# Kernel tuning notes

Hardware: AMD Instinct MI355X
Metric: run time of the kernel (lower is better)

Reference implementation:

```python
import jax, jax.numpy as jnp
import numpy as np

H = 1024
V = 50257
S = 4096
L = 2


def gru_cell(x, h, Wih, Whh, bih, bhh):
    # x: (1, in), h: (1, H); PyTorch GRUCell math
    gi = x @ Wih.T + bih  # (1, 3H)
    gh = h @ Whh.T + bhh  # (1, 3H)
    i_r, i_z, i_n = jnp.split(gi, 3, axis=1)
    h_r, h_z, h_n = jnp.split(gh, 3, axis=1)
    r = jax.nn.sigmoid(i_r + h_r)
    z = jax.nn.sigmoid(i_z + h_z)
    n = jnp.tanh(i_n + r * h_n)
    return (1.0 - z) * n + z * h


def setup_inputs() -> dict:
    key = jax.random.key(0)
    ks = jax.random.split(key, 16)
    s = 0.02
    inp = {
        "input": jax.random.randint(ks[0], (1,), 0, V),
        "last_context": jax.random.normal(ks[1], (1, H), jnp.float32),
        "hidden": jax.random.normal(ks[2], (L, 1, H), jnp.float32),
        "encoder_outputs": jax.random.normal(ks[3], (S, 1, H), jnp.float32),
        "emb": jax.random.normal(ks[4], (V, H), jnp.float32) * s,
        "attn_W": jax.random.normal(ks[5], (H, H), jnp.float32) * s,
        "attn_b": jnp.zeros((H,), jnp.float32),
        "Wih0": jax.random.normal(ks[6], (3 * H, 2 * H), jnp.float32) * s,
        "Whh0": jax.random.normal(ks[7], (3 * H, H), jnp.float32) * s,
        "bih0": jnp.zeros((3 * H,), jnp.float32),
        "bhh0": jnp.zeros((3 * H,), jnp.float32),
        "Wih1": jax.random.normal(ks[8], (3 * H, H), jnp.float32) * s,
        "Whh1": jax.random.normal(ks[9], (3 * H, H), jnp.float32) * s,
        "bih1": jnp.zeros((3 * H,), jnp.float32),
        "bhh1": jnp.zeros((3 * H,), jnp.float32),
        "out_W": jax.random.normal(ks[10], (V, 2 * H), jnp.float32) * s,
        "out_b": jnp.zeros((V,), jnp.float32),
    }
    return inp


def reference(input, last_context, hidden, encoder_outputs, emb, attn_W, attn_b,
              Wih0, Whh0, bih0, bhh0, Wih1, Whh1, bih1, bhh1, out_W, out_b):
    # Embedding lookup for the single decoded token -> (1, H)
    x = emb[input].reshape(1, H)
    rnn_in = jnp.concatenate([x, last_context], axis=1)  # (1, 2H)
    # Stacked 2-layer GRU, single timestep
    h0 = gru_cell(rnn_in, hidden[0], Wih0, Whh0, bih0, bhh0)  # (1, H)
    h1 = gru_cell(h0, hidden[1], Wih1, Whh1, bih1, bhh1)      # (1, H)
    new_hidden = jnp.stack([h0, h1], axis=0)                  # (L, 1, H)
    rnn_output = h1                                           # (1, H)
    # Additive-score attention, vectorized over all S encoder timesteps
    enc = encoder_outputs[:, 0, :]                            # (S, H)
    energies = (enc @ attn_W.T + attn_b) @ rnn_output[0]      # (S,)
    attn_w = jax.nn.softmax(energies)                         # (S,)
    context = (attn_w @ enc).reshape(1, H)                    # (1, H)
    logits = jnp.concatenate([rnn_output, context], axis=1) @ out_W.T + out_b
    output = jax.nn.log_softmax(logits, axis=-1)              # (1, V)
    return output, context, new_hidden, attn_w.reshape(1, 1, S)
```

## Files before the change

kernel.cpp:

```cpp
#include <hip/hip_runtime.h>
#include <math.h>

static constexpr int kH = 1024;
static constexpr int kV = 50257;
static constexpr int kS = 4096;
static constexpr int kLogitsBlocks = (kV + 3) / 4;

__device__ __forceinline__ float wred_sum(float v) {
#pragma unroll
  for (int o = 32; o > 0; o >>= 1) v += __shfl_down(v, o, 64);
  return v;
}
__device__ __forceinline__ float wred_max(float v) {
#pragma unroll
  for (int o = 32; o > 0; o >>= 1) v = fmaxf(v, __shfl_down(v, o, 64));
  return v;
}

__global__ __launch_bounds__(256) void gru_kernel(
    const int* __restrict__ tok, const float* __restrict__ emb,
    const float* __restrict__ xa, const float* __restrict__ xb,
    const float* __restrict__ hprev,
    const float* __restrict__ Wih, const float* __restrict__ Whh,
    const float* __restrict__ bih, const float* __restrict__ bhh,
    float* __restrict__ hout, float* __restrict__ hout2,
    float* __restrict__ zu, float* __restrict__ zc) {
  const int i = blockIdx.x;
  const int t = threadIdx.x;
  const int lane = t & 63, wid = t >> 6;

  if (zu) {
    if (i < 4) zu[i * 256 + t] = 0.f;
    else if (i < 8) zc[(i - 4) * 256 + t] = 0.f;
  }

  const float* xrow = tok ? (emb + (size_t)tok[0] * kH) : xa;
  const int nk4 = tok ? 512 : 256;
  const size_t xw = tok ? (size_t)(2 * kH) : (size_t)kH;

  const float4* X0 = (const float4*)xrow;
  const float4* X1 = (const float4*)xb;
  const float4* Wr = (const float4*)(Wih + (size_t)i * xw);
  const float4* Wz = (const float4*)(Wih + (size_t)(kH + i) * xw);
  const float4* Wn = (const float4*)(Wih + (size_t)(2 * kH + i) * xw);
  const float4* Ur = (const float4*)(Whh + (size_t)i * kH);
  const float4* Uz = (const float4*)(Whh + (size_t)(kH + i) * kH);
  const float4* Un = (const float4*)(Whh + (size_t)(2 * kH + i) * kH);
  const float4* Hp = (const float4*)hprev;

  float ar = 0.f, az = 0.f, an = 0.f, br = 0.f, bz = 0.f, bn = 0.f;
  for (int k = t; k < nk4; k += 256) {
    const float4 x = (k < 256) ? X0[k] : X1[k - 256];
    float4 w;
    w = Wr[k]; ar += w.x * x.x + w.y * x.y + w.z * x.z + w.w * x.w;
    w = Wz[k]; az += w.x * x.x + w.y * x.y + w.z * x.z + w.w * x.w;
    w = Wn[k]; an += w.x * x.x + w.y * x.y + w.z * x.z + w.w * x.w;
  }
  {
    const float4 h = Hp[t];
    float4 w;
    w = Ur[t]; br += w.x * h.x + w.y * h.y + w.z * h.z + w.w * h.w;
    w = Uz[t]; bz += w.x * h.x + w.y * h.y + w.z * h.z + w.w * h.w;
    w = Un[t]; bn += w.x * h.x + w.y * h.y + w.z * h.z + w.w * h.w;
  }
  ar = wred_sum(ar); az = wred_sum(az); an = wred_sum(an);
  br = wred_sum(br); bz = wred_sum(bz); bn = wred_sum(bn);
  __shared__ float red[6][4];
  if (lane == 0) {
    red[0][wid] = ar; red[1][wid] = az; red[2][wid] = an;
    red[3][wid] = br; red[4][wid] = bz; red[5][wid] = bn;
  }
  __syncthreads();
  if (t == 0) {
    const float s0 = red[0][0] + red[0][1] + red[0][2] + red[0][3];
    const float s1 = red[1][0] + red[1][1] + red[1][2] + red[1][3];
    const float s2 = red[2][0] + red[2][1] + red[2][2] + red[2][3];
    const float s3 = red[3][0] + red[3][1] + red[3][2] + red[3][3];
    const float s4 = red[4][0] + red[4][1] + red[4][2] + red[4][3];
    const float s5 = red[5][0] + red[5][1] + red[5][2] + red[5][3];
    const float r = 1.f / (1.f + expf(-((s0 + bih[i]) + (s3 + bhh[i]))));
    const float z = 1.f / (1.f + expf(-((s1 + bih[kH + i]) + (s4 + bhh[kH + i]))));
    const float n = tanhf((s2 + bih[2 * kH + i]) + r * (s5 + bhh[2 * kH + i]));
    const float h = (1.f - z) * n + z * hprev[i];
    hout[i] = h;
    hout2[i] = h;
  }
}

__global__ __launch_bounds__(256) void attn_u_kernel(
    const float* __restrict__ attn_W, const float* __restrict__ h1,
    float* __restrict__ u) {
  const int t = threadIdx.x;
  const int j0 = blockIdx.x * 8;
  const float4* W4 = (const float4*)attn_W;
  float4 acc = make_float4(0.f, 0.f, 0.f, 0.f);
#pragma unroll
  for (int j = j0; j < j0 + 8; ++j) {
    const float hj = h1[j];
    const float4 w = W4[(size_t)j * 256 + t];
    acc.x += hj * w.x; acc.y += hj * w.y; acc.z += hj * w.z; acc.w += hj * w.w;
  }
  atomicAdd(&u[4 * t + 0], acc.x);
  atomicAdd(&u[4 * t + 1], acc.y);
  atomicAdd(&u[4 * t + 2], acc.z);
  atomicAdd(&u[4 * t + 3], acc.w);
}

__global__ __launch_bounds__(256) void energies_kernel(
    const float* __restrict__ enc, const float* __restrict__ u,
    float* __restrict__ e) {
  const int lane = threadIdx.x & 63;
  const int s = blockIdx.x * 4 + (threadIdx.x >> 6);
  const float4* E = (const float4*)(enc + (size_t)s * kH);
  const float4* U = (const float4*)u;
  float acc = 0.f;
#pragma unroll
  for (int k = lane; k < 256; k += 64) {
    const float4 a = E[k], b = U[k];
    acc += a.x * b.x + a.y * b.y + a.z * b.z + a.w * b.w;
  }
  acc = wred_sum(acc);
  if (lane == 0) e[s] = acc;
}

__global__ __launch_bounds__(1024) void softmax4096_kernel(
    float* __restrict__ e, float* __restrict__ o_attn) {
  const int t = threadIdx.x;
  const int lane = t & 63, wid = t >> 6;
  __shared__ float red[16];
  __shared__ float bc;
  const float4 v = ((const float4*)e)[t];
  float m = fmaxf(fmaxf(v.x, v.y), fmaxf(v.z, v.w));
  m = wred_max(m);
  if (lane == 0) red[wid] = m;
  __syncthreads();
  if (t == 0) {
    float mm = red[0];
    for (int w = 1; w < 16; ++w) mm = fmaxf(mm, red[w]);
    bc = mm;
  }
  __syncthreads();
  const float M = bc;
  const float e0 = expf(v.x - M), e1 = expf(v.y - M);
  const float e2 = expf(v.z - M), e3 = expf(v.w - M);
  float ssum = e0 + e1 + e2 + e3;
  ssum = wred_sum(ssum);
  if (lane == 0) red[wid] = ssum;
  __syncthreads();
  if (t == 0) {
    float tt = 0.f;
    for (int w = 0; w < 16; ++w) tt += red[w];
    bc = 1.f / tt;
  }
  __syncthreads();
  const float inv = bc;
  const float4 r4 = make_float4(e0 * inv, e1 * inv, e2 * inv, e3 * inv);
  ((float4*)e)[t] = r4;
  o_attn[4 * t + 0] = r4.x;
  o_attn[4 * t + 1] = r4.y;
  o_attn[4 * t + 2] = r4.z;
  o_attn[4 * t + 3] = r4.w;
}

__global__ __launch_bounds__(256) void context_kernel(
    const float* __restrict__ enc, const float* __restrict__ w,
    float* __restrict__ ctx) {
  const int t = threadIdx.x;
  const int s0 = blockIdx.x * 32;
  const float4* E = (const float4*)enc;
  float4 acc = make_float4(0.f, 0.f, 0.f, 0.f);
#pragma unroll 4
  for (int s = s0; s < s0 + 32; ++s) {
    const float ws = w[s];
    const float4 e = E[(size_t)s * 256 + t];
    acc.x += ws * e.x; acc.y += ws * e.y; acc.z += ws * e.z; acc.w += ws * e.w;
  }
  atomicAdd(&ctx[4 * t + 0], acc.x);
  atomicAdd(&ctx[4 * t + 1], acc.y);
  atomicAdd(&ctx[4 * t + 2], acc.z);
  atomicAdd(&ctx[4 * t + 3], acc.w);
}

__global__ __launch_bounds__(256) void logits_kernel(
    const float* __restrict__ out_W, const float* __restrict__ out_b,
    const float* __restrict__ h1, const float* __restrict__ ctx,
    float* __restrict__ logits, float* __restrict__ part) {
  const int lane = threadIdx.x & 63;
  const int wid = threadIdx.x >> 6;
  const int v = blockIdx.x * 4 + wid;
  __shared__ float lvals[4];

  float val = -INFINITY;
  if (v < kV) {
    const float4* W = (const float4*)(out_W + (size_t)v * (2 * kH));
    const float4* X0 = (const float4*)h1;
    const float4* X1 = (const float4*)ctx;
    float acc = 0.f;
#pragma unroll
    for (int k = lane; k < 512; k += 64) {
      const float4 w = W[k];
      const float4 x = (k < 256) ? X0[k] : X1[k - 256];
      acc += w.x * x.x + w.y * x.y + w.z * x.z + w.w * x.w;
    }
    acc = wred_sum(acc);
    val = acc + out_b[v];
    if (lane == 0) logits[v] = val;
  }
  if (lane == 0) lvals[wid] = val;
  __syncthreads();
  if (threadIdx.x == 0) {
    const float m = fmaxf(fmaxf(lvals[0], lvals[1]), fmaxf(lvals[2], lvals[3]));
    float s = 0.f;
#pragma unroll
    for (int w = 0; w < 4; ++w)
      if (lvals[w] != -INFINITY) s += expf(lvals[w] - m);
    part[2 * blockIdx.x] = m;
    part[2 * blockIdx.x + 1] = s;
  }
}

__global__ __launch_bounds__(1024) void lse_combine_kernel(
    const float* __restrict__ part, float* __restrict__ stats) {
  const int t = threadIdx.x;
  const int lane = t & 63, wid = t >> 6;
  __shared__ float red[16];
  __shared__ float bc;
  float m = -INFINITY;
  for (int b = t; b < kLogitsBlocks; b += 1024) m = fmaxf(m, part[2 * b]);
  m = wred_max(m);
  if (lane == 0) red[wid] = m;
  __syncthreads();
  if (t == 0) {
    float mm = red[0];
    for (int w = 1; w < 16; ++w) mm = fmaxf(mm, red[w]);
    bc = mm;
  }
  __syncthreads();
  const float M = bc;
  float s = 0.f;
  for (int b = t; b < kLogitsBlocks; b += 1024)
    s += part[2 * b + 1] * expf(part[2 * b] - M);
  s = wred_sum(s);
  if (lane == 0) red[wid] = s;
  __syncthreads();
  if (t == 0) {
    float tt = 0.f;
    for (int w = 0; w < 16; ++w) tt += red[w];
    stats[0] = M;
    stats[1] = logf(tt);
  }
}

__global__ __launch_bounds__(256) void finalize_kernel(
    float* __restrict__ logits, const float* __restrict__ stats,
    const float* __restrict__ ctx_ws, float* __restrict__ o_ctx) {
  const int v = blockIdx.x * 256 + threadIdx.x;
  if (v < kV) logits[v] -= (stats[0] + stats[1]);
  if (v < kH) o_ctx[v] = ctx_ws[v];
}

extern "C" void kernel_launch(void* const* d_in, const int* in_sizes, int n_in,
                              void* d_out, int out_size, void* d_ws,
                              size_t ws_size, hipStream_t stream) {
  const int* tok = (const int*)d_in[0];
  const float* last_ctx = (const float*)d_in[1];
  const float* hidden = (const float*)d_in[2];
  const float* enc = (const float*)d_in[3];
  const float* emb = (const float*)d_in[4];
  const float* attn_W = (const float*)d_in[5];
  const float* Wih0 = (const float*)d_in[7];
  const float* Whh0 = (const float*)d_in[8];
  const float* bih0 = (const float*)d_in[9];
  const float* bhh0 = (const float*)d_in[10];
  const float* Wih1 = (const float*)d_in[11];
  const float* Whh1 = (const float*)d_in[12];
  const float* bih1 = (const float*)d_in[13];
  const float* bhh1 = (const float*)d_in[14];
  const float* out_W = (const float*)d_in[15];
  const float* out_b = (const float*)d_in[16];

  float* out = (float*)d_out;
  float* o_logits = out;
  float* o_ctx = out + kV;
  float* o_h0 = out + kV + kH;
  float* o_h1 = out + kV + 2 * kH;
  float* o_attn = out + kV + 3 * kH;

  float* ws_u = (float*)d_ws;
  float* ws_stat = ws_u + kH;
  float* ws_h0 = ws_u + kH + 4;
  float* ws_h1 = ws_h0 + kH;
  float* ws_ctx = ws_h1 + kH;
  float* ws_attn = ws_ctx + kH;
  float* ws_part = ws_attn + kS;

  gru_kernel<<<kH, 256, 0, stream>>>(tok, emb, nullptr, last_ctx, hidden, Wih0,
                                     Whh0, bih0, bhh0, ws_h0, o_h0, ws_u,
                                     ws_ctx);
  gru_kernel<<<kH, 256, 0, stream>>>(nullptr, nullptr, ws_h0, nullptr,
                                     hidden + kH, Wih1, Whh1, bih1, bhh1,
                                     ws_h1, o_h1, nullptr, nullptr);
  attn_u_kernel<<<128, 256, 0, stream>>>(attn_W, ws_h1, ws_u);
  energies_kernel<<<kS / 4, 256, 0, stream>>>(enc, ws_u, ws_attn);
  softmax4096_kernel<<<1, 1024, 0, stream>>>(ws_attn, o_attn);
  context_kernel<<<128, 256, 0, stream>>>(enc, ws_attn, ws_ctx);
  logits_kernel<<<kLogitsBlocks, 256, 0, stream>>>(out_W, out_b, ws_h1, ws_ctx,
                                                   o_logits, ws_part);
  lse_combine_kernel<<<1, 1024, 0, stream>>>(ws_part, ws_stat);
  finalize_kernel<<<(kV + 255) / 256, 256, 0, stream>>>(o_logits, ws_stat,
                                                        ws_ctx, o_ctx);
}
```

Before: 143.2 us.

## Split logits GEMV by halves, fuse softmax into context, merge LSE into finalize

Splits the output projection so the h1 half of out_W is computed alongside the attention u-vector right after the GRU, and only the context half runs after attention. The attention softmax is fused into the context kernel, with each block redundantly recomputing max and sum over 4096 energies. The separate LSE combine kernel is folded into finalize, which now re-reduces 1024 partials in every block. This cuts launches and shortens the serial path after attention, at the cost of redundant reductions and a read-modify-write of the logits.

```diff
diff --git a/kernel.cpp b/kernel.cpp
--- a/kernel.cpp
+++ b/kernel.cpp
@@ -4,7 +4,8 @@
 static constexpr int kH = 1024;
 static constexpr int kV = 50257;
 static constexpr int kS = 4096;
-static constexpr int kLogitsBlocks = (kV + 3) / 4;
+static constexpr int kLogABlocks = (kV + 3) / 4;
+static constexpr int kLogBBlocks = 1024;
 
 __device__ __forceinline__ float wred_sum(float v) {
 #pragma unroll
@@ -87,23 +88,43 @@
   }
 }
 
-__global__ __launch_bounds__(256) void attn_u_kernel(
+__global__ __launch_bounds__(256) void attnu_logitsA_kernel(
     const float* __restrict__ attn_W, const float* __restrict__ h1,
-    float* __restrict__ u) {
-  const int t = threadIdx.x;
-  const int j0 = blockIdx.x * 8;
-  const float4* W4 = (const float4*)attn_W;
-  float4 acc = make_float4(0.f, 0.f, 0.f, 0.f);
-#pragma unroll
-  for (int j = j0; j < j0 + 8; ++j) {
-    const float hj = h1[j];
-    const float4 w = W4[(size_t)j * 256 + t];
-    acc.x += hj * w.x; acc.y += hj * w.y; acc.z += hj * w.z; acc.w += hj * w.w;
-  }
-  atomicAdd(&u[4 * t + 0], acc.x);
-  atomicAdd(&u[4 * t + 1], acc.y);
-  atomicAdd(&u[4 * t + 2], acc.z);
-  atomicAdd(&u[4 * t + 3], acc.w);
+    float* __restrict__ u, const float* __restrict__ out_W,
+    const float* __restrict__ out_b, float* __restrict__ logits) {
+  const int b = blockIdx.x;
+  const int t = threadIdx.x;
+  if (b < 128) {
+    const int j0 = b * 8;
+    const float4* W4 = (const float4*)attn_W;
+    float4 acc = make_float4(0.f, 0.f, 0.f, 0.f);
+#pragma unroll
+    for (int j = j0; j < j0 + 8; ++j) {
+      const float hj = h1[j];
+      const float4 w = W4[(size_t)j * 256 + t];
+      acc.x += hj * w.x; acc.y += hj * w.y;
+      acc.z += hj * w.z; acc.w += hj * w.w;
+    }
+    atomicAdd(&u[4 * t + 0], acc.x);
+    atomicAdd(&u[4 * t + 1], acc.y);
+    atomicAdd(&u[4 * t + 2], acc.z);
+    atomicAdd(&u[4 * t + 3], acc.w);
+    return;
+  }
+  const int lane = t & 63;
+  const int v = (b - 128) * 4 + (t >> 6);
+  if (v >= kV) return;
+  const float4* W = (const float4*)(out_W + (size_t)v * (2 * kH));
+  const float4* X0 = (const float4*)h1;
+  float acc = 0.f;
+#pragma unroll
+  for (int k = lane; k < 256; k += 64) {
+    const float4 w = W[k];
+    const float4 x = X0[k];
+    acc += w.x * x.x + w.y * x.y + w.z * x.z + w.w * x.w;
+  }
+  acc = wred_sum(acc);
+  if (lane == 0) logits[v] = acc + out_b[v];
 }
 
 __global__ __launch_bounds__(256) void energies_kernel(
@@ -123,57 +144,47 @@
   if (lane == 0) e[s] = acc;
 }
 
-__global__ __launch_bounds__(1024) void softmax4096_kernel(
-    float* __restrict__ e, float* __restrict__ o_attn) {
+__global__ __launch_bounds__(256) void softmax_context_kernel(
+    const float* __restrict__ e, const float* __restrict__ enc,
+    float* __restrict__ ctx, float* __restrict__ o_attn) {
+  const int b = blockIdx.x;
   const int t = threadIdx.x;
   const int lane = t & 63, wid = t >> 6;
-  __shared__ float red[16];
-  __shared__ float bc;
-  const float4 v = ((const float4*)e)[t];
-  float m = fmaxf(fmaxf(v.x, v.y), fmaxf(v.z, v.w));
+  __shared__ float red[2][4];
+  __shared__ float bc[2];
+
+  float m = -INFINITY;
+#pragma unroll
+  for (int i = 0; i < 16; ++i) m = fmaxf(m, e[t + 256 * i]);
   m = wred_max(m);
-  if (lane == 0) red[wid] = m;
-  __syncthreads();
-  if (t == 0) {
-    float mm = red[0];
-    for (int w = 1; w < 16; ++w) mm = fmaxf(mm, red[w]);
-    bc = mm;
-  }
-  __syncthreads();
-  const float M = bc;
-  const float e0 = expf(v.x - M), e1 = expf(v.y - M);
-  const float e2 = expf(v.z - M), e3 = expf(v.w - M);
-  float ssum = e0 + e1 + e2 + e3;
-  ssum = wred_sum(ssum);
-  if (lane == 0) red[wid] = ssum;
-  __syncthreads();
-  if (t == 0) {
-    float tt = 0.f;
-    for (int w = 0; w < 16; ++w) tt += red[w];
-    bc = 1.f / tt;
-  }
-  __syncthreads();
-  const float inv = bc;
-  const float4 r4 = make_float4(e0 * inv, e1 * inv, e2 * inv, e3 * inv);
-  ((float4*)e)[t] = r4;
-  o_attn[4 * t + 0] = r4.x;
-  o_attn[4 * t + 1] = r4.y;
-  o_attn[4 * t + 2] = r4.z;
-  o_attn[4 * t + 3] = r4.w;
-}
-
-__global__ __launch_bounds__(256) void context_kernel(
-    const float* __restrict__ enc, const float* __restrict__ w,
-    float* __restrict__ ctx) {
-  const int t = threadIdx.x;
-  const int s0 = blockIdx.x * 32;
-  const float4* E = (const float4*)enc;
+  if (lane == 0) red[0][wid] = m;
+  __syncthreads();
+  if (t == 0)
+    bc[0] = fmaxf(fmaxf(red[0][0], red[0][1]), fmaxf(red[0][2], red[0][3]));
+  __syncthreads();
+  const float M = bc[0];
+  float s = 0.f;
+#pragma unroll
+  for (int i = 0; i < 16; ++i) s += expf(e[t + 256 * i] - M);
+  s = wred_sum(s);
+  if (lane == 0) red[1][wid] = s;
+  __syncthreads();
+  if (t == 0)
+    bc[1] = 1.f / (red[1][0] + red[1][1] + red[1][2] + red[1][3]);
+  __syncthreads();
+  const float invZ = bc[1];
+
+  const int s0 = b * 32;
+  if (t < 32) o_attn[s0 + t] = expf(e[s0 + t] - M) * invZ;
+
+  const float4* E4 = (const float4*)enc;
   float4 acc = make_float4(0.f, 0.f, 0.f, 0.f);
 #pragma unroll 4
-  for (int s = s0; s < s0 + 32; ++s) {
-    const float ws = w[s];
-    const float4 e = E[(size_t)s * 256 + t];
-    acc.x += ws * e.x; acc.y += ws * e.y; acc.z += ws * e.z; acc.w += ws * e.w;
+  for (int si = s0; si < s0 + 32; ++si) {
+    const float wgt = expf(e[si] - M) * invZ;
+    const float4 ev = E4[(size_t)si * 256 + t];
+    acc.x += wgt * ev.x; acc.y += wgt * ev.y;
+    acc.z += wgt * ev.z; acc.w += wgt * ev.w;
   }
   atomicAdd(&ctx[4 * t + 0], acc.x);
   atomicAdd(&ctx[4 * t + 1], acc.y);
@@ -181,82 +192,88 @@
   atomicAdd(&ctx[4 * t + 3], acc.w);
 }
 
-__global__ __launch_bounds__(256) void logits_kernel(
-    const float* __restrict__ out_W, const float* __restrict__ out_b,
-    const float* __restrict__ h1, const float* __restrict__ ctx,
+__global__ __launch_bounds__(256) void logitsB_kernel(
+    const float* __restrict__ out_W, const float* __restrict__ ctx,
     float* __restrict__ logits, float* __restrict__ part) {
-  const int lane = threadIdx.x & 63;
-  const int wid = threadIdx.x >> 6;
-  const int v = blockIdx.x * 4 + wid;
-  __shared__ float lvals[4];
-
-  float val = -INFINITY;
-  if (v < kV) {
-    const float4* W = (const float4*)(out_W + (size_t)v * (2 * kH));
-    const float4* X0 = (const float4*)h1;
-    const float4* X1 = (const float4*)ctx;
-    float acc = 0.f;
-#pragma unroll
-    for (int k = lane; k < 512; k += 64) {
-      const float4 w = W[k];
-      const float4 x = (k < 256) ? X0[k] : X1[k - 256];
-      acc += w.x * x.x + w.y * x.y + w.z * x.z + w.w * x.w;
+  const int b = blockIdx.x;
+  const int t = threadIdx.x;
+  const int lane = t & 63, wid = t >> 6;
+  __shared__ float red[2][4];
+
+  const float4* X1 = (const float4*)ctx;
+  float4 x1[4];
+#pragma unroll
+  for (int j = 0; j < 4; ++j) x1[j] = X1[lane + 64 * j];
+
+  float lm = -INFINITY, ls = 0.f;
+  for (int v = b * 4 + wid; v < kV; v += kLogBBlocks * 4) {
+    const float4* W = (const float4*)(out_W + (size_t)v * (2 * kH)) + 256;
+    float acc1 = 0.f;
+#pragma unroll
+    for (int j = 0; j < 4; ++j) {
+      const float4 w = W[lane + 64 * j];
+      acc1 += w.x * x1[j].x + w.y * x1[j].y + w.z * x1[j].z + w.w * x1[j].w;
     }
-    acc = wred_sum(acc);
-    val = acc + out_b[v];
-    if (lane == 0) logits[v] = val;
-  }
-  if (lane == 0) lvals[wid] = val;
-  __syncthreads();
-  if (threadIdx.x == 0) {
-    const float m = fmaxf(fmaxf(lvals[0], lvals[1]), fmaxf(lvals[2], lvals[3]));
-    float s = 0.f;
-#pragma unroll
-    for (int w = 0; w < 4; ++w)
-      if (lvals[w] != -INFINITY) s += expf(lvals[w] - m);
-    part[2 * blockIdx.x] = m;
-    part[2 * blockIdx.x + 1] = s;
-  }
-}
-
-__global__ __launch_bounds__(1024) void lse_combine_kernel(
-    const float* __restrict__ part, float* __restrict__ stats) {
+    const float acc = wred_sum(acc1);
+    if (lane == 0) {
+      const float val = logits[v] + acc;
+      logits[v] = val;
+      const float M2 = fmaxf(lm, val);
+      ls = ls * expf(lm - M2) + expf(val - M2);
+      lm = M2;
+    }
+  }
+  if (lane == 0) { red[0][wid] = lm; red[1][wid] = ls; }
+  __syncthreads();
+  if (t == 0) {
+    float m = red[0][0], s = red[1][0];
+#pragma unroll
+    for (int w = 1; w < 4; ++w) {
+      const float M2 = fmaxf(m, red[0][w]);
+      s = s * expf(m - M2) + red[1][w] * expf(red[0][w] - M2);
+      m = M2;
+    }
+    part[2 * b] = m;
+    part[2 * b + 1] = s;
+  }
+}
+
+__global__ __launch_bounds__(256) void finalize_kernel(
+    float* __restrict__ logits, const float* __restrict__ part,
+    const float* __restrict__ ctx_ws, float* __restrict__ o_ctx) {
+  const int b = blockIdx.x;
   const int t = threadIdx.x;
   const int lane = t & 63, wid = t >> 6;
-  __shared__ float red[16];
-  __shared__ float bc;
-  float m = -INFINITY;
-  for (int b = t; b < kLogitsBlocks; b += 1024) m = fmaxf(m, part[2 * b]);
-  m = wred_max(m);
-  if (lane == 0) red[wid] = m;
-  __syncthreads();
-  if (t == 0) {
-    float mm = red[0];
-    for (int w = 1; w < 16; ++w) mm = fmaxf(mm, red[w]);
-    bc = mm;
-  }
-  __syncthreads();
-  const float M = bc;
-  float s = 0.f;
-  for (int b = t; b < kLogitsBlocks; b += 1024)
-    s += part[2 * b + 1] * expf(part[2 * b] - M);
-  s = wred_sum(s);
-  if (lane == 0) red[wid] = s;
-  __syncthreads();
-  if (t == 0) {
-    float tt = 0.f;
-    for (int w = 0; w < 16; ++w) tt += red[w];
-    stats[0] = M;
-    stats[1] = logf(tt);
-  }
-}
-
-__global__ __launch_bounds__(256) void finalize_kernel(
-    float* __restrict__ logits, const float* __restrict__ stats,
-    const float* __restrict__ ctx_ws, float* __restrict__ o_ctx) {
-  const int v = blockIdx.x * 256 + threadIdx.x;
-  if (v < kV) logits[v] -= (stats[0] + stats[1]);
-  if (v < kH) o_ctx[v] = ctx_ws[v];
+  __shared__ float red[2][4];
+
+  float m = -INFINITY, s = 0.f;
+  for (int i = t; i < kLogBBlocks; i += 256) {
+    const float bm = part[2 * i], bs = part[2 * i + 1];
+    const float M2 = fmaxf(m, bm);
+    s = s * expf(m - M2) + bs * expf(bm - M2);
+    m = M2;
+  }
+#pragma unroll
+  for (int o = 32; o > 0; o >>= 1) {
+    const float m2 = __shfl_down(m, o, 64);
+    const float s2 = __shfl_down(s, o, 64);
+    const float M2 = fmaxf(m, m2);
+    s = s * expf(m - M2) + s2 * expf(m2 - M2);
+    m = M2;
+  }
+  if (lane == 0) { red[0][wid] = m; red[1][wid] = s; }
+  __syncthreads();
+  float M = red[0][0], S = red[1][0];
+#pragma unroll
+  for (int w = 1; w < 4; ++w) {
+    const float M2 = fmaxf(M, red[0][w]);
+    S = S * expf(M - M2) + red[1][w] * expf(red[0][w] - M2);
+    M = M2;
+  }
+  const float shift = M + logf(S);
+  const int v = b * 256 + t;
+  if (v < kV) logits[v] -= shift;
+  if (b < 4) o_ctx[b * 256 + t] = ctx_ws[b * 256 + t];
 }
 
 extern "C" void kernel_launch(void* const* d_in, const int* in_sizes, int n_in,
@@ -286,13 +303,13 @@
   float* o_h1 = out + kV + 2 * kH;
   float* o_attn = out + kV + 3 * kH;
 
-  float* ws_u = (float*)d_ws;
-  float* ws_stat = ws_u + kH;
-  float* ws_h0 = ws_u + kH + 4;
-  float* ws_h1 = ws_h0 + kH;
-  float* ws_ctx = ws_h1 + kH;
-  float* ws_attn = ws_ctx + kH;
-  float* ws_part = ws_attn + kS;
+  float* ws = (float*)d_ws;
+  float* ws_u = ws;
+  float* ws_h0 = ws + 1024;
+  float* ws_h1 = ws + 2048;
+  float* ws_ctx = ws + 3072;
+  float* ws_attn = ws + 4096;
+  float* ws_part = ws + 8192;
 
   gru_kernel<<<kH, 256, 0, stream>>>(tok, emb, nullptr, last_ctx, hidden, Wih0,
                                      Whh0, bih0, bhh0, ws_h0, o_h0, ws_u,
@@ -300,13 +317,13 @@
   gru_kernel<<<kH, 256, 0, stream>>>(nullptr, nullptr, ws_h0, nullptr,
                                      hidden + kH, Wih1, Whh1, bih1, bhh1,
                                      ws_h1, o_h1, nullptr, nullptr);
-  attn_u_kernel<<<128, 256, 0, stream>>>(attn_W, ws_h1, ws_u);
+  attnu_logitsA_kernel<<<128 + kLogABlocks, 256, 0, stream>>>(
+      attn_W, ws_h1, ws_u, out_W, out_b, o_logits);
   energies_kernel<<<kS / 4, 256, 0, stream>>>(enc, ws_u, ws_attn);
-  softmax4096_kernel<<<1, 1024, 0, stream>>>(ws_attn, o_attn);
-  context_kernel<<<128, 256, 0, stream>>>(enc, ws_attn, ws_ctx);
-  logits_kernel<<<kLogitsBlocks, 256, 0, stream>>>(out_W, out_b, ws_h1, ws_ctx,
-                                                   o_logits, ws_part);
-  lse_combine_kernel<<<1, 1024, 0, stream>>>(ws_part, ws_stat);
-  finalize_kernel<<<(kV + 255) / 256, 256, 0, stream>>>(o_logits, ws_stat,
+  softmax_context_kernel<<<128, 256, 0, stream>>>(ws_attn, enc, ws_ctx,
+                                                  o_attn);
+  logitsB_kernel<<<kLogBBlocks, 256, 0, stream>>>(out_W, ws_ctx, o_logits,
+                                                  ws_part);
+  finalize_kernel<<<(kV + 255) / 256, 256, 0, stream>>>(o_logits, ws_part,
                                                         ws_ctx, o_ctx);
 }
```

After: 131.0 us. -8.6%, faster.
